# Kernel optimization log

Measured on AMD Instinct MI355X. Metric: run time of the kernel, lower is better.

Reference implementation:

```python
import jax, jax.numpy as jnp
import numpy as np

N_TOKEN = 267735
D_EMBED = 1024
D_PROJ = 1024
DIV_VAL = 4
CUTOFFS = [20000, 40000, 200000, N_TOKEN]   # cutoffs + [n_token]
ENDS = [0] + CUTOFFS                         # cutoff_ends
N_CLUSTERS = len(CUTOFFS) - 1                # 3
HEAD_SIZE = CUTOFFS[0] + N_CLUSTERS          # 20003
N = 1024                                     # len*bsz


def setup_inputs() -> dict:
    key = jax.random.key(0)
    ks = jax.random.split(key, 16)
    d_embs = [D_EMBED // DIV_VAL ** i for i in range(4)]  # 1024,256,64,16
    sizes = [HEAD_SIZE] + [ENDS[i + 1] - ENDS[i] for i in range(1, 4)]  # 20003,20000,160000,67735
    s = 0.02
    inp = {
        'hidden': jax.random.normal(ks[0], (N, D_PROJ), dtype=jnp.float32),
        'target': jax.random.randint(ks[1], (N,), 0, N_TOKEN, dtype=jnp.int32),
    }
    for i in range(4):
        inp[f'w{i}'] = jax.random.normal(ks[2 + 3 * i], (sizes[i], d_embs[i]), dtype=jnp.float32) * s
        inp[f'b{i}'] = jnp.zeros((sizes[i],), dtype=jnp.float32)
        inp[f'p{i}'] = jax.random.normal(ks[3 + 3 * i], (D_PROJ, d_embs[i]), dtype=jnp.float32) * s
    return inp


def _logit(h, w, b, p):
    # F.linear(hidden, proj.t()) -> h @ p ; F.linear(., weight, bias) -> @ w.T + b
    return (h @ p) @ w.T + b


def reference(hidden, target, w0, b0, p0, w1, b1, p1, w2, b2, p2, w3, b3, p3):
    head_lp = jax.nn.log_softmax(_logit(hidden, w0, b0, p0), axis=1)  # [N, HEAD_SIZE]
    tails = [(w1, b1, p1), (w2, b2, p2), (w3, b3, p3)]
    lps = []
    # shortlist cluster: gather target logprob directly from head
    t0 = jnp.clip(target, 0, CUTOFFS[0] - 1)
    lps.append(jnp.take_along_axis(head_lp, t0[:, None], axis=1)[:, 0])
    # tail clusters: small projected matmul + log_softmax + gather, combined with cluster logprob head_lp[:, -i]
    for i in range(1, 4):
        l, r = ENDS[i], ENDS[i + 1]
        ti = jnp.clip(target - l, 0, r - l - 1)
        tail_lp = jax.nn.log_softmax(_logit(hidden, *tails[i - 1]), axis=1)  # [N, r-l]
        lps.append(head_lp[:, -i] + jnp.take_along_axis(tail_lp, ti[:, None], axis=1)[:, 0])
    masks = [(target >= ENDS[i]) & (target < ENDS[i + 1]) for i in range(4)]
    logprob = jnp.select(masks, lps)
    return -logprob  # [N] per-token NLL, original order (keep_order=True)
```

## Files before the change

### kernel.cpp

```cpp
#include <hip/hip_runtime.h>
#include <hip/hip_bf16.h>
#include <math.h>

#define NTOK 1024
#define DPROJ 1024
#define PSTRIDE 1376
#define HEADS 20003
#define LOG2E 1.4426950408889634f
#define LN2   0.6931471805599453f
#define WSCALE (4.0f * LOG2E)
#define PSCALE 0.25f

#if __has_builtin(__builtin_amdgcn_exp2f)
#define EXP2(x) __builtin_amdgcn_exp2f(x)
#else
#define EXP2(x) exp2f(x)
#endif

#define MFMA8(a, b, c) __builtin_amdgcn_mfma_f32_16x16x32_fp8_fp8(a, b, c, 0, 0, 0)

typedef __attribute__((ext_vector_type(8))) short bf16x8;
typedef __attribute__((ext_vector_type(4))) float f32x4;
typedef long long i64;
typedef __attribute__((ext_vector_type(2))) long long i64x2;

__device__ __forceinline__ short f2bf(float f) {
    unsigned u = __float_as_uint(f);
    u += 0x7fffu + ((u >> 16) & 1u);
    return (short)(u >> 16);
}
__device__ __forceinline__ unsigned pk4fp8(float a, float b, float c, float d) {
    unsigned v = __builtin_amdgcn_cvt_pk_fp8_f32(a, b, 0, false);
    v = __builtin_amdgcn_cvt_pk_fp8_f32(c, d, v, true);
    return v;
}
__device__ __forceinline__ unsigned char fp8_1(float a) {
    return (unsigned char)(__builtin_amdgcn_cvt_pk_fp8_f32(a, a, 0, false) & 0xff);
}
__device__ __forceinline__ i64 wfrag(const float* wp) {
    float4 x = *(const float4*)(wp);
    float4 y = *(const float4*)(wp + 4);
    unsigned lo = pk4fp8(x.x * WSCALE, x.y * WSCALE, x.z * WSCALE, x.w * WSCALE);
    unsigned hi = pk4fp8(y.x * WSCALE, y.y * WSCALE, y.z * WSCALE, y.w * WSCALE);
    return (i64)(((unsigned long long)hi << 32) | lo);
}

#define NB0H 313
#define NB1T 157
#define NB2T 313
#define NB3T 133
#define NSLAB (NB0H + NB1T + NB2T + NB3T)

#define EB0N 20096
#define EB1N 20096
#define EB2N 160256
#define EB3N 68096
#define EBTOT (EB0N + EB1N + EB2N + EB3N)

__global__ __launch_bounds__(256) void prep(const float* __restrict__ hidden,
                                            const float* __restrict__ p0,
                                            const float* __restrict__ p1,
                                            const float* __restrict__ p2,
                                            const float* __restrict__ p3,
                                            const float* __restrict__ b0,
                                            const float* __restrict__ b1,
                                            const float* __restrict__ b2,
                                            const float* __restrict__ b3,
                                            short* __restrict__ hbP,
                                            short* __restrict__ pTbP0,
                                            short* __restrict__ pTbP1,
                                            short* __restrict__ pTbP2,
                                            short* __restrict__ pTbP3,
                                            float* __restrict__ sums,
                                            unsigned char* __restrict__ pk3,
                                            float* __restrict__ eb0,
                                            float* __restrict__ eb1,
                                            float* __restrict__ eb2,
                                            float* __restrict__ eb3) {
    __shared__ float tile[64][65];
    int bid = blockIdx.x, tid = threadIdx.x;
    if (bid >= 418) {
        int g = (bid - 418) * 256 + tid;
        if (g < EB0N) {
            eb0[g] = (g < HEADS) ? exp2f(b0[g] * LOG2E) : 0.f;
        } else if (g < EB0N + EB1N) {
            int i = g - EB0N;
            eb1[i] = (i < 20000) ? exp2f(b1[i] * LOG2E) : 0.f;
        } else if (g < EB0N + EB1N + EB2N) {
            int i = g - EB0N - EB1N;
            eb2[i] = (i < 160000) ? exp2f(b2[i] * LOG2E) : 0.f;
        } else if (g < EBTOT) {
            int i = g - EB0N - EB1N - EB2N;
            eb3[i] = (i < 67735) ? exp2f(b3[i] * LOG2E) : 0.f;
        }
        return;
    }
    if (bid == 416) {
        float4 z = {0.f, 0.f, 0.f, 0.f};
        #pragma unroll
        for (int i = 0; i < 4; ++i) *((float4*)sums + i * 256 + tid) = z;
        return;
    }
    if (bid == 417) {
        int4 z = {0, 0, 0, 0};
        #pragma unroll
        for (int i = 0; i < 8; ++i) *((int4*)pk3 + i * 256 + tid) = z;
        return;
    }
    if (bid < 64) {
        int tt = bid;
        #pragma unroll
        for (int q = 0; q < 8; ++q) {
            int fi = q * 256 + tid;
            int l = fi & 63;
            int row = tt * 16 + (l & 15);
            int kb = (fi >> 6) * 32 + (l >> 4) * 8;
            const float* hp = hidden + row * 1024 + kb;
            float4 x = *(const float4*)hp;
            float4 y = *(const float4*)(hp + 4);
            bf16x8 o;
            o[0]=f2bf(x.x); o[1]=f2bf(x.y); o[2]=f2bf(x.z); o[3]=f2bf(x.w);
            o[4]=f2bf(y.x); o[5]=f2bf(y.y); o[6]=f2bf(y.z); o[7]=f2bf(y.w);
            *(bf16x8*)(hbP + (size_t)tt * 16384 + fi * 8) = o;
        }
        return;
    }
    int lb = bid - 64;
    const float* p; short* dst; int d, kt, jb;
    if (lb < 256)      { p = p0; dst = pTbP0; d = 1024; kt = lb >> 4; jb = lb & 15; }
    else if (lb < 320) { lb -= 256; p = p1; dst = pTbP1; d = 256; kt = lb >> 2; jb = lb & 3; }
    else if (lb < 336) { lb -= 320; p = p2; dst = pTbP2; d = 64;  kt = lb; jb = 0; }
    else               { lb -= 336; p = p3; dst = pTbP3; d = 16;  kt = lb; jb = 0; }
    int k0 = kt * 64, j0 = jb * 64;
    int tx = tid & 63, ty = tid >> 6;
    #pragma unroll
    for (int rr = 0; rr < 16; ++rr) {
        int k = k0 + ty * 16 + rr;
        int j = j0 + tx;
        if (j < d) tile[ty * 16 + rr][tx] = p[k * d + j];
    }
    __syncthreads();
    int ch = tid >> 5;
    int jtl = ch >> 1, ksl = ch & 1;
    int jt = jb * 4 + jtl;
    if (jt * 16 < d) {
        #pragma unroll
        for (int li = 0; li < 2; ++li) {
            int l = (tid & 31) + li * 32;
            int jl = jtl * 16 + (l & 15);
            int kl = ksl * 32 + (l >> 4) * 8;
            bf16x8 o;
            #pragma unroll
            for (int e = 0; e < 8; ++e) o[e] = f2bf(tile[kl + e][jl]);
            *(bf16x8*)(dst + ((size_t)jt * 32 + kt * 2 + ksl) * 512 + l * 8) = o;
        }
    }
}

__global__ __launch_bounds__(256) void proj(const short* __restrict__ hbP,
                                            const short* __restrict__ pTbP0,
                                            const short* __restrict__ pTbP1,
                                            const short* __restrict__ pTbP2,
                                            const short* __restrict__ pTbP3,
                                            float* __restrict__ projf,
                                            unsigned char* __restrict__ pk0,
                                            unsigned char* __restrict__ pk1,
                                            unsigned char* __restrict__ pk2,
                                            unsigned char* __restrict__ pk3) {
    __shared__ float spackf[16][72];
    __shared__ unsigned char sp8[1024];
    int tt = blockIdx.x, jbG = blockIdx.y, tid = threadIdx.x;
    const short* pB; unsigned char* pkc; int d, KSp, coloff, jb;
    if (jbG < 16)      { pB = pTbP0; pkc = pk0; d = 1024; KSp = 32; coloff = 0;    jb = jbG; }
    else if (jbG < 20) { pB = pTbP1; pkc = pk1; d = 256;  KSp = 8;  coloff = 1024; jb = jbG - 16; }
    else if (jbG == 20){ pB = pTbP2; pkc = pk2; d = 64;   KSp = 2;  coloff = 1280; jb = 0; }
    else               { pB = pTbP3; pkc = pk3; d = 16;   KSp = 1;  coloff = 1344; jb = 0; }
    int w = tid >> 6, lane = tid & 63;
    int l16 = lane & 15, quad = lane >> 4;
    int jt = jb * 4 + w;
    if (jt * 16 < d) {
        const short* ap = hbP + ((size_t)tt * 32) * 512 + lane * 8;
        const short* bp = pB  + ((size_t)jt * 32) * 512 + lane * 8;
        f32x4 x0 = {0,0,0,0}, x1 = {0,0,0,0};
        #pragma unroll
        for (int ks = 0; ks < 16; ++ks) {
            bf16x8 a0 = *(const bf16x8*)(ap + ks * 512);
            bf16x8 b0 = *(const bf16x8*)(bp + ks * 512);
            bf16x8 a1 = *(const bf16x8*)(ap + (ks + 16) * 512);
            bf16x8 b1 = *(const bf16x8*)(bp + (ks + 16) * 512);
            x0 = __builtin_amdgcn_mfma_f32_16x16x32_bf16(a0, b0, x0, 0, 0, 0);
            x1 = __builtin_amdgcn_mfma_f32_16x16x32_bf16(a1, b1, x1, 0, 0, 0);
        }
        f32x4 acc = x0 + x1;
        int kk = w * 16 + l16;
        #pragma unroll
        for (int r = 0; r < 4; ++r) {
            int tok = quad * 4 + r;
            spackf[tok][kk] = acc[r];
            int idx;
            if (d > 16) idx = ((kk & 31) >> 3) * 256 + tok * 16 + (kk >> 5) * 8 + (kk & 7);
            else        idx = ((kk & 31) >> 3) * 128 + tok * 8 + (kk & 7);
            sp8[idx] = fp8_1(acc[r] * PSCALE);
        }
    }
    __syncthreads();
    int j0g = jb * 64;
    int dcols = min(64, d - j0g);
    {
        int row = tid >> 4, cb = (tid & 15) * 4;
        if (cb < dcols) {
            float4 v = *(const float4*)&spackf[row][cb];
            *(float4*)&projf[(tt * 16 + row) * PSTRIDE + coloff + j0g + cb] = v;
        }
    }
    {
        int nbytes = 16 * dcols;
        if (tid * 4 < nbytes) {
            unsigned char* gdst = pkc + ((size_t)tt * KSp + (j0g >> 5)) * 512;
            *(unsigned*)(gdst + tid * 4) = *(const unsigned*)(sp8 + tid * 4);
        }
    }
}

__device__ __forceinline__ void stage16k(const unsigned char* g, unsigned char* l,
                                         int wave, int lane) {
    const unsigned char* gs = g + wave * 4096 + lane * 16;
    unsigned char* ls = l + wave * 4096;
    #pragma unroll
    for (int i = 0; i < 4; ++i)
        __builtin_amdgcn_global_load_lds(
            (const __attribute__((address_space(1))) unsigned*)(gs + i * 1024),
            (__attribute__((address_space(3))) unsigned*)(ls + i * 1024), 16, 0, 0);
}

__device__ __forceinline__ void lse_head(const float* __restrict__ w,
                                         const float* __restrict__ eb,
                                         const unsigned char* __restrict__ pk,
                                         float* __restrict__ part, int bid,
                                         unsigned char (*sbuf)[16384], float* bsum) {
    int tid = threadIdx.x;
    int wave = tid >> 6, lane = tid & 63;
    int quad = lane >> 4, l16 = lane & 15;
    int v0 = bid * 64 + wave * 16;

    for (int i = tid; i < NTOK; i += 256) bsum[i] = 0.f;

    i64 areg[32];
    float ee[4];
    int va = v0 + l16;
    #pragma unroll
    for (int ks = 0; ks < 32; ++ks)
        areg[ks] = (va < HEADS) ? wfrag(w + (long)va * 1024 + ks * 32 + quad * 8) : 0;
    #pragma unroll
    for (int r = 0; r < 4; ++r)
        ee[r] = eb[v0 + quad * 4 + r];

    stage16k(pk, sbuf[0], wave, lane);
    __syncthreads();
    for (int tt = 0; tt < 64; ++tt) {
        if (tt < 63) stage16k(pk + (size_t)(tt + 1) * 16384, sbuf[(tt + 1) & 1], wave, lane);
        const unsigned char* sb = sbuf[tt & 1];
        f32x4 x0 = {0,0,0,0}, x1 = x0;
        __builtin_amdgcn_s_setprio(1);
        #pragma unroll
        for (int p = 0; p < 16; ++p) {
            i64x2 b2 = *(const i64x2*)(sb + p * 1024 + lane * 16);
            x0 = MFMA8(areg[2 * p],     b2[0], x0);
            x1 = MFMA8(areg[2 * p + 1], b2[1], x1);
        }
        __builtin_amdgcn_s_setprio(0);
        f32x4 a = x0 + x1;
        float e0 = EXP2(a[0]) * ee[0] + EXP2(a[2]) * ee[2];
        float e1 = EXP2(a[1]) * ee[1] + EXP2(a[3]) * ee[3];
        float e = e0 + e1;
        e += __shfl_xor(e, 16, 64);
        e += __shfl_xor(e, 32, 64);
        if (lane < 16) atomicAdd(&bsum[tt * 16 + lane], e);
        __syncthreads();
    }
    *((float4*)part + tid) = *((const float4*)bsum + tid);
}

template <int KS, int VT>
__device__ __forceinline__ void lse_tail(const float* __restrict__ w,
                                         const float* __restrict__ eb,
                                         const unsigned char* __restrict__ pk,
                                         float* __restrict__ part,
                                         int V, int D, int bid, float* bsum) {
    int tid = threadIdx.x;
    int wave = tid >> 6, lane = tid & 63;
    int quad = lane >> 4, l16 = lane & 15;
    int v0 = bid * (64 * VT) + wave * (16 * VT);

    for (int i = tid; i < NTOK; i += 256) bsum[i] = 0.f;
    __syncthreads();

    i64 areg[VT][KS];
    float ee[VT][4];
    #pragma unroll
    for (int vt = 0; vt < VT; ++vt) {
        int va = v0 + vt * 16 + l16;
        #pragma unroll
        for (int ks = 0; ks < KS; ++ks) {
            int k = ks * 32 + quad * 8;
            areg[vt][ks] = (va < V && k < D) ? wfrag(w + (long)va * D + k) : 0;
        }
        #pragma unroll
        for (int r = 0; r < 4; ++r)
            ee[vt][r] = eb[v0 + vt * 16 + quad * 4 + r];
    }

    if constexpr (KS >= 2) {
        constexpr int KSP = KS / 2;
        i64x2 bn[KSP], bc[KSP];
        #pragma unroll
        for (int p = 0; p < KSP; ++p)
            bn[p] = *(const i64x2*)(pk + p * 1024 + lane * 16);
        for (int tt = 0; tt < 64; ++tt) {
            #pragma unroll
            for (int p = 0; p < KSP; ++p) bc[p] = bn[p];
            if (tt < 63) {
                const unsigned char* nb = pk + (size_t)(tt + 1) * (KS * 512);
                #pragma unroll
                for (int p = 0; p < KSP; ++p)
                    bn[p] = *(const i64x2*)(nb + p * 1024 + lane * 16);
            }
            float e0 = 0.f, e1 = 0.f;
            #pragma unroll
            for (int vt = 0; vt < VT; ++vt) {
                f32x4 y0 = {0,0,0,0}, y1 = {0,0,0,0};
                __builtin_amdgcn_s_setprio(1);
                #pragma unroll
                for (int p = 0; p < KSP; ++p) {
                    y0 = MFMA8(areg[vt][2 * p],     bc[p][0], y0);
                    y1 = MFMA8(areg[vt][2 * p + 1], bc[p][1], y1);
                }
                __builtin_amdgcn_s_setprio(0);
                f32x4 a = y0 + y1;
                e0 += EXP2(a[0]) * ee[vt][0];
                e1 += EXP2(a[1]) * ee[vt][1];
                e0 += EXP2(a[2]) * ee[vt][2];
                e1 += EXP2(a[3]) * ee[vt][3];
            }
            float e = e0 + e1;
            e += __shfl_xor(e, 16, 64);
            e += __shfl_xor(e, 32, 64);
            if (lane < 16) atomicAdd(&bsum[tt * 16 + lane], e);
        }
    } else {
        i64 bn = *(const i64*)(pk + lane * 8);
        for (int tt = 0; tt < 64; ++tt) {
            i64 bc = bn;
            if (tt < 63) bn = *(const i64*)(pk + (size_t)(tt + 1) * 512 + lane * 8);
            float e0 = 0.f, e1 = 0.f;
            #pragma unroll
            for (int vt = 0; vt < VT; ++vt) {
                f32x4 y0 = {0,0,0,0};
                f32x4 a = MFMA8(areg[vt][0], bc, y0);
                e0 += EXP2(a[0]) * ee[vt][0];
                e1 += EXP2(a[1]) * ee[vt][1];
                e0 += EXP2(a[2]) * ee[vt][2];
                e1 += EXP2(a[3]) * ee[vt][3];
            }
            float e = e0 + e1;
            e += __shfl_xor(e, 16, 64);
            e += __shfl_xor(e, 32, 64);
            if (lane < 16) atomicAdd(&bsum[tt * 16 + lane], e);
        }
    }
    __syncthreads();
    *((float4*)part + tid) = *((const float4*)bsum + tid);
}

__global__ __launch_bounds__(256, 2) void lse_all(const float* __restrict__ w0, const float* __restrict__ eb0,
                                                  const float* __restrict__ w1, const float* __restrict__ eb1,
                                                  const float* __restrict__ w2, const float* __restrict__ eb2,
                                                  const float* __restrict__ w3, const float* __restrict__ eb3,
                                                  const unsigned char* __restrict__ pk0,
                                                  const unsigned char* __restrict__ pk1,
                                                  const unsigned char* __restrict__ pk2,
                                                  const unsigned char* __restrict__ pk3,
                                                  float* __restrict__ part) {
    __shared__ unsigned char sbuf[2][16384];
    __shared__ float bsum[NTOK];
    int bid = blockIdx.x;
    float* slab = part + (size_t)bid * NTOK;
    if (bid < NB0H) {
        lse_head(w0, eb0, pk0, slab, bid, sbuf, bsum);
    } else if (bid < NB0H + NB1T) {
        lse_tail<8, 2>(w1, eb1, pk1, slab, 20000,  256, bid - NB0H, bsum);
    } else if (bid < NB0H + NB1T + NB2T) {
        lse_tail<2, 8>(w2, eb2, pk2, slab, 160000, 64,  bid - NB0H - NB1T, bsum);
    } else {
        lse_tail<1, 8>(w3, eb3, pk3, slab, 67735,  16,  bid - NB0H - NB1T - NB2T, bsum);
    }
}

__global__ __launch_bounds__(256) void reduce_part(const float* __restrict__ part,
                                                   float* __restrict__ sums) {
    int bid = blockIdx.x;
    int c = bid >> 5, rem = bid & 31, q = rem >> 3, sl = rem & 7;
    const int off[4] = {0, NB0H, NB0H + NB1T, NB0H + NB1T + NB2T};
    const int cnt[4] = {NB0H, NB1T, NB2T, NB3T};
    int tok = q * 256 + threadIdx.x;
    const float* p = part + (size_t)off[c] * NTOK + tok;
    int n = cnt[c];
    float s0 = 0.f, s1 = 0.f, s2 = 0.f, s3 = 0.f;
    int b = sl;
    for (; b + 24 < n; b += 32) {
        s0 += p[(size_t)b * NTOK];
        s1 += p[(size_t)(b + 8) * NTOK];
        s2 += p[(size_t)(b + 16) * NTOK];
        s3 += p[(size_t)(b + 24) * NTOK];
    }
    for (; b < n; b += 8) s0 += p[(size_t)b * NTOK];
    float s = (s0 + s1) + (s2 + s3);
    atomicAdd(&sums[c * NTOK + tok], s);
}

__global__ __launch_bounds__(256) void finalize(const int* __restrict__ target,
                                                const float* __restrict__ projf,
                                                const float* __restrict__ sums,
                                                const float* __restrict__ w0, const float* __restrict__ b0,
                                                const float* __restrict__ w1, const float* __restrict__ b1,
                                                const float* __restrict__ w2, const float* __restrict__ b2,
                                                const float* __restrict__ w3, const float* __restrict__ b3,
                                                float* __restrict__ out) {
    int wave = threadIdx.x >> 6, lane = threadIdx.x & 63;
    int row = blockIdx.x * 4 + wave;
    int t = target[row];
    int c = (t < 20000) ? 0 : (t < 40000) ? 1 : (t < 200000) ? 2 : 3;
    int col0 = (c == 0) ? t : (HEADS - c);
    const float* pr = projf + row * PSTRIDE;

    float s = 0.f;
    for (int k = lane; k < DPROJ; k += 64) s += pr[k] * w0[col0 * DPROJ + k];
    #pragma unroll
    for (int off = 32; off; off >>= 1) s += __shfl_xor(s, off, 64);
    float hl = s + b0[col0];
    float lse0 = __log2f(sums[row]) * LN2;

    float res;
    if (c == 0) {
        res = lse0 - hl;
    } else {
        const float* wc; const float* bc; int d, coloff, l;
        if (c == 1)      { wc = w1; bc = b1; d = 256; coloff = 1024; l = 20000; }
        else if (c == 2) { wc = w2; bc = b2; d = 64;  coloff = 1280; l = 40000; }
        else             { wc = w3; bc = b3; d = 16;  coloff = 1344; l = 200000; }
        int tc = t - l;
        float s2 = 0.f;
        for (int k = lane; k < d; k += 64) s2 += pr[coloff + k] * wc[tc * d + k];
        #pragma unroll
        for (int off = 32; off; off >>= 1) s2 += __shfl_xor(s2, off, 64);
        float tl = s2 + bc[tc];
        float lsec = __log2f(sums[c * NTOK + row]) * LN2;
        res = lse0 - hl + lsec - tl;
    }
    if (lane == 0) out[row] = res;
}


extern "C" void kernel_launch(void* const* d_in, const int* in_sizes, int n_in,
                              void* d_out, int out_size, void* d_ws, size_t ws_size,
                              hipStream_t stream) {
    const float* hidden = (const float*)d_in[0];
    const int*   target = (const int*)d_in[1];
    const float* w0 = (const float*)d_in[2];
    const float* b0 = (const float*)d_in[3];
    const float* p0 = (const float*)d_in[4];
    const float* w1 = (const float*)d_in[5];
    const float* b1 = (const float*)d_in[6];
    const float* p1 = (const float*)d_in[7];
    const float* w2 = (const float*)d_in[8];
    const float* b2 = (const float*)d_in[9];
    const float* p2 = (const float*)d_in[10];
    const float* w3 = (const float*)d_in[11];
    const float* b3 = (const float*)d_in[12];
    const float* p3 = (const float*)d_in[13];

    short* base = (short*)d_ws;
    short* hbP   = base;
    short* pTbP0 = base + 1048576;
    short* pTbP1 = base + 2097152;
    short* pTbP2 = base + 2359296;
    short* pTbP3 = base + 2424832;
    float* projf = (float*)((char*)d_ws + 4882432);
    unsigned char* pk0 = (unsigned char*)d_ws + 10518528;
    unsigned char* pk1 = pk0 + 1048576;
    unsigned char* pk2 = pk1 + 262144;
    unsigned char* pk3 = pk2 + 65536;
    float* sums  = (float*)((char*)d_ws + 11927552);
    float* part  = (float*)((char*)d_ws + 11943936);
    float* eb0   = (float*)((char*)d_ws + 15695872);
    float* eb1   = (float*)((char*)d_ws + 15776256);
    float* eb2   = (float*)((char*)d_ws + 15856640);
    float* eb3   = (float*)((char*)d_ws + 16497664);

    prep<<<1467, 256, 0, stream>>>(hidden, p0, p1, p2, p3, b0, b1, b2, b3,
                                   hbP, pTbP0, pTbP1, pTbP2, pTbP3, sums, pk3,
                                   eb0, eb1, eb2, eb3);
    proj<<<dim3(64, 22), 256, 0, stream>>>(hbP, pTbP0, pTbP1, pTbP2, pTbP3,
                                           projf, pk0, pk1, pk2, pk3);
    lse_all<<<NSLAB, 256, 0, stream>>>(w0, eb0, w1, eb1, w2, eb2, w3, eb3,
                                       pk0, pk1, pk2, pk3, part);
    reduce_part<<<128, 256, 0, stream>>>(part, sums);
    finalize<<<256, 256, 0, stream>>>(target, projf, sums,
                                      w0, b0, w1, b1, w2, b2, w3, b3, (float*)d_out);
}
```

Measured before the change: 310.6 us.

## Triple-buffer head LDS staging and batch tail MFMAs before exp

The head path goes from double to triple buffering of the 16 KB LDS staging buffers, so the stage two tiles ahead overlaps with compute. The tail paths now issue all MFMAs for every vocab subtile first at raised priority, then run the exp2/scale work, which gives the scheduler independent matrix ops to interleave. The cost is 16 KB more LDS per block (about 53 KB total), which may limit occupancy under launch_bounds(256,2), plus higher register pressure from the held accumulators.

New measurement: 305.1 us. Within noise of the previous version (-1.8%).

```diff
diff --git a/kernel.cpp b/kernel.cpp
--- a/kernel.cpp
+++ b/kernel.cpp
@@ -255,11 +255,15 @@
     for (int r = 0; r < 4; ++r)
         ee[r] = eb[v0 + quad * 4 + r];
 
-    stage16k(pk, sbuf[0], wave, lane);
+    unsigned char* pA = sbuf[0];
+    unsigned char* pB = sbuf[1];
+    unsigned char* pS = sbuf[2];
+    stage16k(pk, pA, wave, lane);
+    stage16k(pk + 16384, pB, wave, lane);
     __syncthreads();
     for (int tt = 0; tt < 64; ++tt) {
-        if (tt < 63) stage16k(pk + (size_t)(tt + 1) * 16384, sbuf[(tt + 1) & 1], wave, lane);
-        const unsigned char* sb = sbuf[tt & 1];
+        if (tt + 2 < 64) stage16k(pk + (size_t)(tt + 2) * 16384, pS, wave, lane);
+        const unsigned char* sb = pA;
         f32x4 x0 = {0,0,0,0}, x1 = x0;
         __builtin_amdgcn_s_setprio(1);
         #pragma unroll
@@ -277,6 +281,7 @@
         e += __shfl_xor(e, 32, 64);
         if (lane < 16) atomicAdd(&bsum[tt * 16 + lane], e);
         __syncthreads();
+        unsigned char* t = pA; pA = pB; pB = pS; pS = t;
     }
     *((float4*)part + tid) = *((const float4*)bsum + tid);
 }
@@ -325,22 +330,33 @@
                 for (int p = 0; p < KSP; ++p)
                     bn[p] = *(const i64x2*)(nb + p * 1024 + lane * 16);
             }
+            f32x4 accs[VT];
+            __builtin_amdgcn_s_setprio(1);
+            #pragma unroll
+            for (int vt = 0; vt < VT; ++vt) {
+                if constexpr (KS >= 4) {
+                    f32x4 y0 = {0,0,0,0}, y1 = {0,0,0,0};
+                    #pragma unroll
+                    for (int p = 0; p < KSP; ++p) {
+                        y0 = MFMA8(areg[vt][2 * p],     bc[p][0], y0);
+                        y1 = MFMA8(areg[vt][2 * p + 1], bc[p][1], y1);
+                    }
+                    accs[vt] = y0 + y1;
+                } else {
+                    f32x4 y = {0,0,0,0};
+                    y = MFMA8(areg[vt][0], bc[0][0], y);
+                    y = MFMA8(areg[vt][1], bc[0][1], y);
+                    accs[vt] = y;
+                }
+            }
+            __builtin_amdgcn_s_setprio(0);
             float e0 = 0.f, e1 = 0.f;
             #pragma unroll
             for (int vt = 0; vt < VT; ++vt) {
-                f32x4 y0 = {0,0,0,0}, y1 = {0,0,0,0};
-                __builtin_amdgcn_s_setprio(1);
-                #pragma unroll
-                for (int p = 0; p < KSP; ++p) {
-                    y0 = MFMA8(areg[vt][2 * p],     bc[p][0], y0);
-                    y1 = MFMA8(areg[vt][2 * p + 1], bc[p][1], y1);
-                }
-                __builtin_amdgcn_s_setprio(0);
-                f32x4 a = y0 + y1;
-                e0 += EXP2(a[0]) * ee[vt][0];
-                e1 += EXP2(a[1]) * ee[vt][1];
-                e0 += EXP2(a[2]) * ee[vt][2];
-                e1 += EXP2(a[3]) * ee[vt][3];
+                e0 += EXP2(accs[vt][0]) * ee[vt][0];
+                e1 += EXP2(accs[vt][1]) * ee[vt][1];
+                e0 += EXP2(accs[vt][2]) * ee[vt][2];
+                e1 += EXP2(accs[vt][3]) * ee[vt][3];
             }
             float e = e0 + e1;
             e += __shfl_xor(e, 16, 64);
@@ -352,15 +368,21 @@
         for (int tt = 0; tt < 64; ++tt) {
             i64 bc = bn;
             if (tt < 63) bn = *(const i64*)(pk + (size_t)(tt + 1) * 512 + lane * 8);
+            f32x4 accs[VT];
+            __builtin_amdgcn_s_setprio(1);
+            #pragma unroll
+            for (int vt = 0; vt < VT; ++vt) {
+                f32x4 y0 = {0,0,0,0};
+                accs[vt] = MFMA8(areg[vt][0], bc, y0);
+            }
+            __builtin_amdgcn_s_setprio(0);
             float e0 = 0.f, e1 = 0.f;
             #pragma unroll
             for (int vt = 0; vt < VT; ++vt) {
-                f32x4 y0 = {0,0,0,0};
-                f32x4 a = MFMA8(areg[vt][0], bc, y0);
-                e0 += EXP2(a[0]) * ee[vt][0];
-                e1 += EXP2(a[1]) * ee[vt][1];
-                e0 += EXP2(a[2]) * ee[vt][2];
-                e1 += EXP2(a[3]) * ee[vt][3];
+                e0 += EXP2(accs[vt][0]) * ee[vt][0];
+                e1 += EXP2(accs[vt][1]) * ee[vt][1];
+                e0 += EXP2(accs[vt][2]) * ee[vt][2];
+                e1 += EXP2(accs[vt][3]) * ee[vt][3];
             }
             float e = e0 + e1;
             e += __shfl_xor(e, 16, 64);
@@ -381,7 +403,7 @@
                                                   const unsigned char* __restrict__ pk2,
                                                   const unsigned char* __restrict__ pk3,
                                                   float* __restrict__ part) {
-    __shared__ unsigned char sbuf[2][16384];
+    __shared__ unsigned char sbuf[3][16384];
     __shared__ float bsum[NTOK];
     int bid = blockIdx.x;
     float* slab = part + (size_t)bid * NTOK;
```
